# Kernel optimization log

Measured on AMD Instinct MI355X. Metric: run time of the kernel, lower is better.

The kernel has to match this reference:

```python
import jax, jax.numpy as jnp
import numpy as np

B, D, C = 16384, 1024, 2048

def setup_inputs() -> dict:
    key = jax.random.key(0)
    k1, k2 = jax.random.split(key)
    x = jax.random.normal(k1, (B, D), dtype=jnp.float32)
    # kaiming_normal_ with nonlinearity='relu': std = sqrt(2 / fan_in)
    W = jax.random.normal(k2, (C, D), dtype=jnp.float32) * jnp.sqrt(2.0 / D)
    return {"x": x, "W": W, "task_id": 0}

def reference(x, W, task_id):
    # Original: -(x[:, :, None] - W.T[None, :, :])**2 .mean(1)  -> [B, C]
    # Algebraic rewrite: -(||x||^2/D - 2*x.W^T/D + ||w||^2/D)
    d = jnp.asarray(x.shape[1], x.dtype)
    x2 = jnp.sum(x * x, axis=1, keepdims=True) / d          # [B, 1]
    w2 = jnp.sum(W * W, axis=1) / d                          # [C]
    cross = jnp.einsum('bd,cd->bc', x, W) * (2.0 / d)        # [B, C]
    return cross - x2 - w2[None, :]
```

## Files before the change

kernel.cpp:

```cpp
#include <hip/hip_runtime.h>
#include <hip/hip_bf16.h>
#include <stdint.h>

#define B_ROWS 16384
#define D_DIM  1024
#define C_DIM  2048
#define KT32   (D_DIM / 32)

typedef short bf16x8 __attribute__((ext_vector_type(8)));
typedef float f32x4  __attribute__((ext_vector_type(4)));
typedef unsigned short us4 __attribute__((ext_vector_type(4)));

#define AS1 __attribute__((address_space(1)))
#define AS3 __attribute__((address_space(3)))
#define BARRIER __builtin_amdgcn_s_barrier()
#define LGKM0 asm volatile("s_waitcnt lgkmcnt(0)")
#define VMCNT(n) asm volatile("s_waitcnt vmcnt(" #n ")" ::: "memory")
#define PRIO1 __builtin_amdgcn_s_setprio(1)
#define PRIO0 __builtin_amdgcn_s_setprio(0)

__device__ __forceinline__ float sq4(f32x4 v) {
    return v[0]*v[0] + v[1]*v[1] + v[2]*v[2] + v[3]*v[3];
}

__global__ __launch_bounds__(256) void pack_rows(
        const float* __restrict__ x, const float* __restrict__ W,
        ushort* __restrict__ Abf, ushort* __restrict__ Bbf,
        float* __restrict__ x2, float* __restrict__ w2) {
    int row = blockIdx.x * 4 + (threadIdx.x >> 6);
    const int lane = threadIdx.x & 63;
    const float* src; ushort* dst; float* norm;
    if (row < B_ROWS) { src = x; dst = Abf; norm = x2; }
    else { row -= B_ROWS; src = W; dst = Bbf; norm = w2; }

    const float* rp = src + (size_t)row * D_DIM;
    ushort*      wp = dst + (size_t)row * D_DIM;

    float s = 0.f;
    #pragma unroll
    for (int p = 0; p < 4; ++p) {
        const int o = (p * 64 + lane) * 4;
        const f32x4 v = *(const f32x4*)(rp + o);
        s += sq4(v);
        ushort u[4]; __hip_bfloat16 h;
        h = __float2bfloat16(v[0]); u[0] = *(const ushort*)&h;
        h = __float2bfloat16(v[1]); u[1] = *(const ushort*)&h;
        h = __float2bfloat16(v[2]); u[2] = *(const ushort*)&h;
        h = __float2bfloat16(v[3]); u[3] = *(const ushort*)&h;
        *(us4*)(wp + o) = *(const us4*)u;
    }
    s += __shfl_xor(s, 1,  64);
    s += __shfl_xor(s, 2,  64);
    s += __shfl_xor(s, 4,  64);
    s += __shfl_xor(s, 8,  64);
    s += __shfl_xor(s, 16, 64);
    s += __shfl_xor(s, 32, 64);
    if (lane == 0) norm[row] = s * (1.0f / (float)D_DIM);
}

__global__ __launch_bounds__(256, 3) void gemm_tb(
        const ushort* __restrict__ Abf, const ushort* __restrict__ Bbf,
        const float* __restrict__ x2, const float* __restrict__ w2,
        float* __restrict__ out) {
    __shared__ ushort As[3 * 4096];
    __shared__ ushort Bs[3 * 4096];

    const int tid  = threadIdx.x;
    const int lane = tid & 63;
    const int wv   = tid >> 6;

    const int wid = (blockIdx.x & 7) * 256 + (blockIdx.x >> 3);
    const int bm  = wid >> 4;
    const int bn  = wid & 15;

    const ushort* aSrc = Abf + (size_t)(bm * 128 + (lane & 15)) * D_DIM + (lane >> 4) * 8;
    const ushort* bSrc = Bbf + (size_t)(bn * 128 + (lane & 15)) * D_DIM + (lane >> 4) * 8;

    const ushort* aRd = As + (wv >> 1) * 2048 + lane * 8;
    const ushort* bRd = Bs + (wv & 1) * 2048 + lane * 8;

    const int t0 = wv, t1 = wv + 4;

#define STAGE(ktc, bufO) do { \
    __builtin_amdgcn_global_load_lds( \
        (const AS1 void*)(aSrc + (size_t)t0 * 16 * D_DIM + (ktc) * 32), \
        (AS3 void*)(As + (bufO) + t0 * 512), 16, 0, 0); \
    __builtin_amdgcn_global_load_lds( \
        (const AS1 void*)(aSrc + (size_t)t1 * 16 * D_DIM + (ktc) * 32), \
        (AS3 void*)(As + (bufO) + t1 * 512), 16, 0, 0); \
    __builtin_amdgcn_global_load_lds( \
        (const AS1 void*)(bSrc + (size_t)t0 * 16 * D_DIM + (ktc) * 32), \
        (AS3 void*)(Bs + (bufO) + t0 * 512), 16, 0, 0); \
    __builtin_amdgcn_global_load_lds( \
        (const AS1 void*)(bSrc + (size_t)t1 * 16 * D_DIM + (ktc) * 32), \
        (AS3 void*)(Bs + (bufO) + t1 * 512), 16, 0, 0); \
  } while (0)

    f32x4 acc[4][4];
    #pragma unroll
    for (int mi = 0; mi < 4; ++mi)
        #pragma unroll
        for (int ni = 0; ni < 4; ++ni)
            acc[mi][ni] = (f32x4){0.f, 0.f, 0.f, 0.f};

    STAGE(0, 0);
    STAGE(1, 4096);
    VMCNT(4);
    BARRIER;

    int curO = 0, nxtO = 4096, stgO = 8192;
    for (int kt = 0; kt < KT32; ++kt) {
        bf16x8 a[4], b[4];
        #pragma unroll
        for (int mi = 0; mi < 4; ++mi)
            a[mi] = *(const bf16x8*)(aRd + curO + mi * 512);
        #pragma unroll
        for (int ni = 0; ni < 4; ++ni)
            b[ni] = *(const bf16x8*)(bRd + curO + ni * 512);

        STAGE((kt + 2) & 31, stgO);

        VMCNT(4);
        BARRIER;
        LGKM0;
        PRIO1;
        #pragma unroll
        for (int mi = 0; mi < 4; ++mi)
            #pragma unroll
            for (int ni = 0; ni < 4; ++ni)
                acc[mi][ni] = __builtin_amdgcn_mfma_f32_16x16x32_bf16(
                    a[mi], b[ni], acc[mi][ni], 0, 0, 0);
        PRIO0;
        BARRIER;

        const int t = curO; curO = nxtO; nxtO = stgO; stgO = t;
    }

    const float scale = 2.0f / (float)D_DIM;
    const int rsel = lane & 15;
    const int quad = lane >> 4;
    const int mT0  = bm * 8 + (wv >> 1) * 4;
    const int nT0  = bn * 8 + (wv & 1) * 4;
    const int row0 = mT0 * 16 + quad * 4;
    const int col0 = nT0 * 16 + rsel;

    float x2r[4][4];
    #pragma unroll
    for (int mi = 0; mi < 4; ++mi)
        #pragma unroll
        for (int r = 0; r < 4; ++r)
            x2r[mi][r] = x2[row0 + mi * 16 + r];

    #pragma unroll
    for (int ni = 0; ni < 4; ++ni) {
        const int c = col0 + ni * 16;
        const float wc = w2[c];
        #pragma unroll
        for (int mi = 0; mi < 4; ++mi) {
            #pragma unroll
            for (int r = 0; r < 4; ++r) {
                const int rr = row0 + mi * 16 + r;
                out[(size_t)rr * C_DIM + c] = acc[mi][ni][r] * scale - x2r[mi][r] - wc;
            }
        }
    }
#undef STAGE
}

extern "C" void kernel_launch(void* const* d_in, const int* in_sizes, int n_in,
                              void* d_out, int out_size, void* d_ws, size_t ws_size,
                              hipStream_t stream) {
    const float* x = (const float*)d_in[0];
    const float* W = (const float*)d_in[1];
    float* out = (float*)d_out;

    char* ws = (char*)d_ws;
    ushort* Abf = (ushort*)ws;
    ushort* Bbf = (ushort*)(ws + (size_t)B_ROWS * D_DIM * sizeof(ushort));
    float*  x2  = (float*)(ws + (size_t)(B_ROWS + C_DIM) * D_DIM * sizeof(ushort));
    float*  w2  = x2 + B_ROWS;

    pack_rows<<<(B_ROWS + C_DIM) / 4, 256, 0, stream>>>(
        x, W, Abf, Bbf, x2, w2);

    gemm_tb<<<(B_ROWS / 128) * (C_DIM / 128), 256, 0, stream>>>(
        Abf, Bbf, x2, w2, out);
}
```

Before: 306.6 us.

## Fuse x bf16 conversion and row norms into GEMM, pre-tile W

Drops the separate pass that converted x to bf16 and computed its row norms. The GEMM now streams fp32 x tiles directly into XOR-swizzled LDS, converts them to bf16 in registers, and accumulates the x row norms inside the K loop. W is packed into an MFMA-ready tiled layout with norms accumulated by atomics, so the write and re-read of a 32 MB bf16 copy of x is avoided. The cost is twice the LDS traffic and footprint for A, occupancy lowered from 3 to 2 blocks, conversion work on the critical path, and x re-read in fp32 by each of the 16 column blocks.

```diff
diff --git a/kernel.cpp b/kernel.cpp
--- a/kernel.cpp
+++ b/kernel.cpp
@@ -6,10 +6,10 @@
 #define D_DIM  1024
 #define C_DIM  2048
 #define KT32   (D_DIM / 32)
+#define NT_TOT (C_DIM  / 16)
 
 typedef short bf16x8 __attribute__((ext_vector_type(8)));
 typedef float f32x4  __attribute__((ext_vector_type(4)));
-typedef unsigned short us4 __attribute__((ext_vector_type(4)));
 
 #define AS1 __attribute__((address_space(1)))
 #define AS3 __attribute__((address_space(3)))
@@ -23,47 +23,43 @@
     return v[0]*v[0] + v[1]*v[1] + v[2]*v[2] + v[3]*v[3];
 }
 
-__global__ __launch_bounds__(256) void pack_rows(
-        const float* __restrict__ x, const float* __restrict__ W,
-        ushort* __restrict__ Abf, ushort* __restrict__ Bbf,
-        float* __restrict__ x2, float* __restrict__ w2) {
-    int row = blockIdx.x * 4 + (threadIdx.x >> 6);
-    const int lane = threadIdx.x & 63;
-    const float* src; ushort* dst; float* norm;
-    if (row < B_ROWS) { src = x; dst = Abf; norm = x2; }
-    else { row -= B_ROWS; src = W; dst = Bbf; norm = w2; }
-
-    const float* rp = src + (size_t)row * D_DIM;
-    ushort*      wp = dst + (size_t)row * D_DIM;
-
-    float s = 0.f;
-    #pragma unroll
-    for (int p = 0; p < 4; ++p) {
-        const int o = (p * 64 + lane) * 4;
-        const f32x4 v = *(const f32x4*)(rp + o);
-        s += sq4(v);
-        ushort u[4]; __hip_bfloat16 h;
-        h = __float2bfloat16(v[0]); u[0] = *(const ushort*)&h;
-        h = __float2bfloat16(v[1]); u[1] = *(const ushort*)&h;
-        h = __float2bfloat16(v[2]); u[2] = *(const ushort*)&h;
-        h = __float2bfloat16(v[3]); u[3] = *(const ushort*)&h;
-        *(us4*)(wp + o) = *(const us4*)u;
-    }
-    s += __shfl_xor(s, 1,  64);
-    s += __shfl_xor(s, 2,  64);
-    s += __shfl_xor(s, 4,  64);
-    s += __shfl_xor(s, 8,  64);
+__device__ __forceinline__ bf16x8 pk8v(f32x4 lo, f32x4 hi) {
+    ushort u[8]; __hip_bfloat16 h;
+    h = __float2bfloat16(lo[0]); u[0] = *(const ushort*)&h;
+    h = __float2bfloat16(lo[1]); u[1] = *(const ushort*)&h;
+    h = __float2bfloat16(lo[2]); u[2] = *(const ushort*)&h;
+    h = __float2bfloat16(lo[3]); u[3] = *(const ushort*)&h;
+    h = __float2bfloat16(hi[0]); u[4] = *(const ushort*)&h;
+    h = __float2bfloat16(hi[1]); u[5] = *(const ushort*)&h;
+    h = __float2bfloat16(hi[2]); u[6] = *(const ushort*)&h;
+    h = __float2bfloat16(hi[3]); u[7] = *(const ushort*)&h;
+    return *(const bf16x8*)u;
+}
+
+__global__ __launch_bounds__(256) void pack_w(
+        const float* __restrict__ W, ushort* __restrict__ Bpk,
+        float* __restrict__ w2) {
+    const int chunk = blockIdx.x * 4 + (threadIdx.x >> 6);
+    const int lane  = threadIdx.x & 63;
+    const int tile  = chunk >> 5;
+    const int kt    = chunk & 31;
+    const int row   = tile * 16 + (lane & 15);
+    const int k0    = kt * 32 + (lane >> 4) * 8;
+    const f32x4 v0 = *(const f32x4*)(W + (size_t)row * D_DIM + k0);
+    const f32x4 v1 = *(const f32x4*)(W + (size_t)row * D_DIM + k0 + 4);
+    float s = sq4(v0) + sq4(v1);
+    *(bf16x8*)(Bpk + ((size_t)chunk * 64 + lane) * 8) = pk8v(v0, v1);
     s += __shfl_xor(s, 16, 64);
     s += __shfl_xor(s, 32, 64);
-    if (lane == 0) norm[row] = s * (1.0f / (float)D_DIM);
-}
-
-__global__ __launch_bounds__(256, 3) void gemm_tb(
-        const ushort* __restrict__ Abf, const ushort* __restrict__ Bbf,
-        const float* __restrict__ x2, const float* __restrict__ w2,
-        float* __restrict__ out) {
-    __shared__ ushort As[3 * 4096];
+    if (lane < 16) atomicAdd(w2 + tile * 16 + lane, s * (1.0f / (float)D_DIM));
+}
+
+__global__ __launch_bounds__(256, 2) void gemm_af32(
+        const float* __restrict__ x, const ushort* __restrict__ Bpk,
+        const float* __restrict__ w2, float* __restrict__ out) {
+    __shared__ float  As[3 * 4096];
     __shared__ ushort Bs[3 * 4096];
+    __shared__ float  nx[128];
 
     const int tid  = threadIdx.x;
     const int lane = tid & 63;
@@ -73,27 +69,27 @@
     const int bm  = wid >> 4;
     const int bn  = wid & 15;
 
-    const ushort* aSrc = Abf + (size_t)(bm * 128 + (lane & 15)) * D_DIM + (lane >> 4) * 8;
-    const ushort* bSrc = Bbf + (size_t)(bn * 128 + (lane & 15)) * D_DIM + (lane >> 4) * 8;
-
-    const ushort* aRd = As + (wv >> 1) * 2048 + lane * 8;
-    const ushort* bRd = Bs + (wv & 1) * 2048 + lane * 8;
-
-    const int t0 = wv, t1 = wv + 4;
-
-#define STAGE(ktc, bufO) do { \
-    __builtin_amdgcn_global_load_lds( \
-        (const AS1 void*)(aSrc + (size_t)t0 * 16 * D_DIM + (ktc) * 32), \
-        (AS3 void*)(As + (bufO) + t0 * 512), 16, 0, 0); \
-    __builtin_amdgcn_global_load_lds( \
-        (const AS1 void*)(aSrc + (size_t)t1 * 16 * D_DIM + (ktc) * 32), \
-        (AS3 void*)(As + (bufO) + t1 * 512), 16, 0, 0); \
-    __builtin_amdgcn_global_load_lds( \
-        (const AS1 void*)(bSrc + (size_t)t0 * 16 * D_DIM + (ktc) * 32), \
-        (AS3 void*)(Bs + (bufO) + t0 * 512), 16, 0, 0); \
-    __builtin_amdgcn_global_load_lds( \
-        (const AS1 void*)(bSrc + (size_t)t1 * 16 * D_DIM + (ktc) * 32), \
-        (AS3 void*)(Bs + (bufO) + t1 * 512), 16, 0, 0); \
+    const float* aStage = x + (size_t)(bm * 128 + (lane >> 3)) * D_DIM
+                            + ((lane & 7) ^ (lane >> 3)) * 4;
+    const ushort* bStage = Bpk + ((size_t)(bn * 8) * KT32) * 512 + lane * 8;
+
+    const int r = lane & 15;
+    const int q = lane >> 4;
+    const int aLo = r * 32 + (((2 * q) ^ (r & 7)) * 4);
+    const int aHi = aLo ^ 4;
+    const float*  aRdL = As + (wv >> 1) * 2048 + aLo;
+    const float*  aRdH = As + (wv >> 1) * 2048 + aHi;
+    const ushort* bRd  = Bs + (wv & 1) * 2048 + lane * 8;
+
+#define GLL(src, dst) __builtin_amdgcn_global_load_lds( \
+        (const AS1 void*)(src), (AS3 void*)(dst), 16, 0, 0)
+#define STAGE(ktc, s) do { \
+    GLL(aStage + (size_t)(wv * 16 + 0)       * D_DIM + (ktc) * 32, As + (s) * 4096 + wv * 512); \
+    GLL(aStage + (size_t)(wv * 16 + 8)       * D_DIM + (ktc) * 32, As + (s) * 4096 + wv * 512 + 256); \
+    GLL(aStage + (size_t)((wv + 4) * 16 + 0) * D_DIM + (ktc) * 32, As + (s) * 4096 + (wv + 4) * 512); \
+    GLL(aStage + (size_t)((wv + 4) * 16 + 8) * D_DIM + (ktc) * 32, As + (s) * 4096 + (wv + 4) * 512 + 256); \
+    GLL(bStage + ((size_t)wv       * KT32 + (ktc)) * 512, Bs + (s) * 4096 + wv * 512); \
+    GLL(bStage + ((size_t)(wv + 4) * KT32 + (ktc)) * 512, Bs + (s) * 4096 + (wv + 4) * 512); \
   } while (0)
 
     f32x4 acc[4][4];
@@ -102,27 +98,38 @@
         #pragma unroll
         for (int ni = 0; ni < 4; ++ni)
             acc[mi][ni] = (f32x4){0.f, 0.f, 0.f, 0.f};
+    float nxa[4] = {0.f, 0.f, 0.f, 0.f};
 
     STAGE(0, 0);
-    STAGE(1, 4096);
-    VMCNT(4);
+    STAGE(1, 1);
+    VMCNT(6);
     BARRIER;
 
-    int curO = 0, nxtO = 4096, stgO = 8192;
+    int cur = 0, nxt = 1, stg = 2;
     for (int kt = 0; kt < KT32; ++kt) {
-        bf16x8 a[4], b[4];
-        #pragma unroll
-        for (int mi = 0; mi < 4; ++mi)
-            a[mi] = *(const bf16x8*)(aRd + curO + mi * 512);
+        f32x4 al[4], ah[4]; bf16x8 b[4];
+        #pragma unroll
+        for (int mi = 0; mi < 4; ++mi) {
+            al[mi] = *(const f32x4*)(aRdL + cur * 4096 + mi * 512);
+            ah[mi] = *(const f32x4*)(aRdH + cur * 4096 + mi * 512);
+        }
         #pragma unroll
         for (int ni = 0; ni < 4; ++ni)
-            b[ni] = *(const bf16x8*)(bRd + curO + ni * 512);
-
-        STAGE((kt + 2) & 31, stgO);
-
-        VMCNT(4);
+            b[ni] = *(const bf16x8*)(bRd + cur * 4096 + ni * 512);
+
+        STAGE((kt + 2) & 31, stg);
+
+        VMCNT(6);
         BARRIER;
         LGKM0;
+
+        bf16x8 a[4];
+        #pragma unroll
+        for (int mi = 0; mi < 4; ++mi) {
+            nxa[mi] += sq4(al[mi]) + sq4(ah[mi]);
+            a[mi] = pk8v(al[mi], ah[mi]);
+        }
+
         PRIO1;
         #pragma unroll
         for (int mi = 0; mi < 4; ++mi)
@@ -133,23 +140,33 @@
         PRIO0;
         BARRIER;
 
-        const int t = curO; curO = nxtO; nxtO = stgO; stgO = t;
+        const int t = cur; cur = nxt; nxt = stg; stg = t;
     }
+
+    const float inv = 1.0f / (float)D_DIM;
+    #pragma unroll
+    for (int mi = 0; mi < 4; ++mi) {
+        float s = nxa[mi] * inv;
+        s += __shfl_xor(s, 16, 64);
+        s += __shfl_xor(s, 32, 64);
+        if (!(wv & 1) && lane < 16)
+            nx[(wv >> 1) * 64 + mi * 16 + lane] = s;
+    }
+    __syncthreads();
 
     const float scale = 2.0f / (float)D_DIM;
     const int rsel = lane & 15;
     const int quad = lane >> 4;
-    const int mT0  = bm * 8 + (wv >> 1) * 4;
-    const int nT0  = bn * 8 + (wv & 1) * 4;
-    const int row0 = mT0 * 16 + quad * 4;
-    const int col0 = nT0 * 16 + rsel;
+    const int lr0  = (wv >> 1) * 64 + quad * 4;
+    const int row0 = bm * 128 + lr0;
+    const int col0 = bn * 128 + (wv & 1) * 64 + rsel;
 
     float x2r[4][4];
     #pragma unroll
     for (int mi = 0; mi < 4; ++mi)
         #pragma unroll
-        for (int r = 0; r < 4; ++r)
-            x2r[mi][r] = x2[row0 + mi * 16 + r];
+        for (int rr = 0; rr < 4; ++rr)
+            x2r[mi][rr] = nx[lr0 + mi * 16 + rr];
 
     #pragma unroll
     for (int ni = 0; ni < 4; ++ni) {
@@ -158,13 +175,14 @@
         #pragma unroll
         for (int mi = 0; mi < 4; ++mi) {
             #pragma unroll
-            for (int r = 0; r < 4; ++r) {
-                const int rr = row0 + mi * 16 + r;
-                out[(size_t)rr * C_DIM + c] = acc[mi][ni][r] * scale - x2r[mi][r] - wc;
+            for (int rr = 0; rr < 4; ++rr) {
+                const int gr = row0 + mi * 16 + rr;
+                out[(size_t)gr * C_DIM + c] = acc[mi][ni][rr] * scale - x2r[mi][rr] - wc;
             }
         }
     }
 #undef STAGE
+#undef GLL
 }
 
 extern "C" void kernel_launch(void* const* d_in, const int* in_sizes, int n_in,
@@ -175,14 +193,13 @@
     float* out = (float*)d_out;
 
     char* ws = (char*)d_ws;
-    ushort* Abf = (ushort*)ws;
-    ushort* Bbf = (ushort*)(ws + (size_t)B_ROWS * D_DIM * sizeof(ushort));
-    float*  x2  = (float*)(ws + (size_t)(B_ROWS + C_DIM) * D_DIM * sizeof(ushort));
-    float*  w2  = x2 + B_ROWS;
-
-    pack_rows<<<(B_ROWS + C_DIM) / 4, 256, 0, stream>>>(
-        x, W, Abf, Bbf, x2, w2);
-
-    gemm_tb<<<(B_ROWS / 128) * (C_DIM / 128), 256, 0, stream>>>(
-        Abf, Bbf, x2, w2, out);
-}
+    ushort* Bpk = (ushort*)ws;
+    float*  w2  = (float*)(ws + (size_t)C_DIM * D_DIM * sizeof(ushort));
+
+    hipMemsetAsync(w2, 0, C_DIM * sizeof(float), stream);
+
+    pack_w<<<NT_TOT * KT32 / 4, 256, 0, stream>>>(W, Bpk, w2);
+
+    gemm_af32<<<(B_ROWS / 128) * (C_DIM / 128), 256, 0, stream>>>(
+        x, Bpk, w2, out);
+}
```

Result: faster. 289.9 us (-5.5%).
